# Kernel optimization log

Measured on AMD Instinct MI355X. Metric: run time of the kernel, lower is better.

The kernel has to match this reference:

```python
import jax, jax.numpy as jnp
import numpy as np

B, C, H, W = 16, 256, 64, 64
NH, AG = 8, 64
KD = C // NH
N = H * W


def _bn_params(k, ch):
    k1, k2, k3, k4 = jax.random.split(k, 4)
    g = 1.0 + 0.1 * jax.random.normal(k1, (ch,), jnp.float32)
    b = 0.1 * jax.random.normal(k2, (ch,), jnp.float32)
    m = 0.1 * jax.random.normal(k3, (ch,), jnp.float32)
    v = jax.random.uniform(k4, (ch,), jnp.float32, 0.5, 1.5)
    return jnp.stack([g, b, m, v])


def setup_inputs() -> dict:
    key = jax.random.key(0)
    ks = jax.random.split(key, 16)
    return {
        "x": jax.random.normal(ks[0], (B, C, H, W), jnp.float32),
        "qkv_w": 0.05 * jax.random.normal(ks[1], (3 * C, C), jnp.float32),
        "qkv_bn": _bn_params(ks[2], 3 * C),
        "pe_w": 0.1 * jax.random.normal(ks[3], (C, 1, 3, 3), jnp.float32),
        "pe_bn": _bn_params(ks[4], C),
        "proj_w": 0.05 * jax.random.normal(ks[5], (C, C), jnp.float32),
        "proj_bn": _bn_params(ks[6], C),
        "an_bias": 0.02 * jax.random.normal(ks[7], (NH, AG, 7, 7), jnp.float32),
        "na_bias": 0.02 * jax.random.normal(ks[8], (NH, AG, 7, 7), jnp.float32),
        "ah_bias": 0.02 * jax.random.normal(ks[9], (1, NH, AG, H, 1), jnp.float32),
        "aw_bias": 0.02 * jax.random.normal(ks[10], (1, NH, AG, 1, W), jnp.float32),
        "ha_bias": 0.02 * jax.random.normal(ks[11], (1, NH, H, 1, AG), jnp.float32),
        "wa_bias": 0.02 * jax.random.normal(ks[12], (1, NH, 1, W, AG), jnp.float32),
    }


def _bn(x, p):
    # inference batchnorm: p = [gamma, beta, running_mean, running_var], eps=1e-5
    g, b, m, v = p
    inv = g * jax.lax.rsqrt(v + 1e-5)
    return (x - m[:, None, None]) * inv[:, None, None] + b[:, None, None]


def reference(x, qkv_w, qkv_bn, pe_w, pe_bn, proj_w, proj_bn,
              an_bias, na_bias, ah_bias, aw_bias, ha_bias, wa_bias):
    scale = KD ** -0.5
    qkv = _bn(jnp.einsum('bchw,oc->bohw', x, qkv_w), qkv_bn)  # [B,3C,H,W]
    qkv = qkv.reshape(B, NH, 3 * KD, N)
    q, k, v = qkv[:, :, :KD], qkv[:, :, KD:2 * KD], qkv[:, :, 2 * KD:]  # [B,NH,KD,N]
    # agent tokens: torch's raw reshape of q to [B,H,W,C], NCHW permute, adaptive avg pool to 8x8
    ps = int(AG ** 0.5)
    ap = q.reshape(B, H, W, C).transpose(0, 3, 1, 2)
    ap = ap.reshape(B, C, ps, H // ps, ps, W // ps).mean(axis=(3, 5)).reshape(B, C, AG)
    a = ap.transpose(0, 2, 1).reshape(B, AG, NH, KD).transpose(0, 2, 3, 1)  # [B,NH,KD,AG]
    # agent -> key attention with interpolated + separable position bias
    pb = (jax.image.resize(an_bias, (NH, AG, H, W), 'bilinear').reshape(1, NH, AG, N)
          + (ah_bias + aw_bias).reshape(1, NH, AG, N))
    attn_k = jax.nn.softmax(jnp.einsum('bhca,bhcn->bhan', a, k) * scale + pb, axis=-1)
    attn = jnp.einsum('bhan,bhcn->bhac', attn_k, v)  # [B,NH,AG,KD]
    # query -> agent attention
    ab = (jax.image.resize(na_bias, (NH, AG, H, W), 'bilinear').reshape(1, NH, AG, N).transpose(0, 1, 3, 2)
          + (ha_bias + wa_bias).reshape(1, NH, N, AG))
    q_attn = jax.nn.softmax(jnp.einsum('bhcn,bhca->bhna', q, a) * scale + ab, axis=-1)
    out = jnp.einsum('bhna,bhac->bhcn', q_attn, attn).reshape(B, C, H, W)
    # depthwise 3x3 positional conv on v + residual
    pe = jax.lax.conv_general_dilated(v.reshape(B, C, H, W), pe_w, (1, 1), 'SAME',
                                      feature_group_count=C,
                                      dimension_numbers=('NCHW', 'OIHW', 'NCHW'))
    out = out + _bn(pe, pe_bn)
    return _bn(jnp.einsum('bchw,oc->bohw', out, proj_w), proj_bn)
```

## Files before the change

kernel.cpp:

```cpp
#include <hip/hip_runtime.h>
#include <cmath>


typedef __bf16 bf16;
typedef bf16 bf16x8 __attribute__((ext_vector_type(8)));
typedef float f32x4 __attribute__((ext_vector_type(4)));

__device__ __forceinline__ f32x4 MFMA16(bf16x8 a, bf16x8 b, f32x4 c) {
  return __builtin_amdgcn_mfma_f32_16x16x32_bf16(a, b, c, 0, 0, 0);
}

__device__ __forceinline__ void gll16(const bf16* g, bf16* l) {
  __builtin_amdgcn_global_load_lds(
      (const __attribute__((address_space(1))) void*)g,
      (__attribute__((address_space(3))) void*)l, 16, 0, 0);
}

constexpr int B_ = 16, C_ = 256, N_ = 4096;
constexpr int NH_ = 8, KD_ = 32, AG_ = 64, O3_ = 768;
constexpr int PSTRIDE_ = 64 + 64 + 64 * 32;
constexpr float SCALE_ = 0.17677669529663687f;

__global__ __launch_bounds__(256) void prep_w_kernel(
    const float* __restrict__ qkv_w, const float* __restrict__ qkv_bn,
    const float* __restrict__ proj_w, const float* __restrict__ proj_bn,
    bf16* __restrict__ wqb, float* __restrict__ shq,
    bf16* __restrict__ wpb, float* __restrict__ shp) {
  int o = blockIdx.x, t = threadIdx.x;
  if (o < O3_) {
    float g = qkv_bn[o], bb = qkv_bn[O3_ + o], m = qkv_bn[2 * O3_ + o],
          v = qkv_bn[3 * O3_ + o];
    float s = g * rsqrtf(v + 1e-5f);
    wqb[(size_t)o * C_ + t] = (bf16)(qkv_w[(size_t)o * C_ + t] * s);
    if (t == 0) shq[o] = bb - m * s;
  } else {
    int p = o - O3_;
    float g = proj_bn[p], bb = proj_bn[C_ + p], m = proj_bn[2 * C_ + p],
          v = proj_bn[3 * C_ + p];
    float s = g * rsqrtf(v + 1e-5f);
    wpb[(size_t)p * C_ + t] = (bf16)(proj_w[(size_t)p * C_ + t] * s);
    if (t == 0) shp[p] = bb - m * s;
  }
}

__device__ __forceinline__ float bilerp7(const float* __restrict__ A, int h, int w) {
  float fy = (h + 0.5f) * (7.0f / 64.0f) - 0.5f;
  float fx = (w + 0.5f) * (7.0f / 64.0f) - 0.5f;
  float fy0 = floorf(fy), fx0 = floorf(fx);
  float wy = fy - fy0, wx = fx - fx0;
  int y0 = (int)fy0, x0 = (int)fx0;
  int y0c = min(max(y0, 0), 6), y1c = min(max(y0 + 1, 0), 6);
  int x0c = min(max(x0, 0), 6), x1c = min(max(x0 + 1, 0), 6);
  float a00 = A[y0c * 7 + x0c], a01 = A[y0c * 7 + x1c];
  float a10 = A[y1c * 7 + x0c], a11 = A[y1c * 7 + x1c];
  return (1.0f - wy) * ((1.0f - wx) * a00 + wx * a01) +
         wy * ((1.0f - wx) * a10 + wx * a11);
}

__global__ __launch_bounds__(256) void bias_pb_kernel(
    const float* __restrict__ an, const float* __restrict__ ah,
    const float* __restrict__ aw, bf16* __restrict__ pb) {
  int tid = blockIdx.x * 256 + threadIdx.x;
  int n = tid & (N_ - 1);
  int g = (tid >> 12) & 63;
  int nh = tid >> 18;
  int h = n >> 6, w = n & 63;
  float v = bilerp7(an + (nh * AG_ + g) * 49, h, w);
  pb[tid] = (bf16)(v + ah[(nh * AG_ + g) * 64 + h] + aw[(nh * AG_ + g) * 64 + w]);
}

__global__ __launch_bounds__(256) void bias_ab_kernel(
    const float* __restrict__ na, const float* __restrict__ ha,
    const float* __restrict__ wa, bf16* __restrict__ ab) {
  int tid = blockIdx.x * 256 + threadIdx.x;
  int g = tid & 63;
  int n = (tid >> 6) & (N_ - 1);
  int nh = tid >> 18;
  int h = n >> 6, w = n & 63;
  float v = bilerp7(na + (nh * AG_ + g) * 49, h, w);
  ab[tid] = (bf16)(v + ha[(nh * 64 + h) * AG_ + g] + wa[(nh * 64 + w) * AG_ + g]);
}

__global__ __launch_bounds__(256) void transpose_x_kernel(
    const float* __restrict__ x, bf16* __restrict__ xT) {
  __shared__ __align__(16) unsigned LDSd[64 * 36];
  int b = blockIdx.x, n0 = blockIdx.y * 64, c0 = blockIdx.z * 64;
  int t = threadIdx.x, n = t & 63, cp = t >> 6;
  const float* xb = x + ((size_t)b * C_ + c0) * N_ + n0;
#pragma unroll
  for (int j = 0; j < 8; j++) {
    int cpr = cp * 8 + j;
    int c = cpr * 2;
    float f0 = xb[(size_t)c * N_ + n];
    float f1 = xb[(size_t)(c + 1) * N_ + n];
    union { bf16 h[2]; unsigned u; } pk;
    pk.h[0] = (bf16)f0; pk.h[1] = (bf16)f1;
    LDSd[n * 36 + cpr] = pk.u;
  }
  __syncthreads();
  int n2 = t >> 2, seg = t & 3;
  const unsigned* row = &LDSd[n2 * 36 + seg * 8];
  uint4 d0 = *(const uint4*)row;
  uint4 d1 = *(const uint4*)(row + 4);
  bf16* dst = xT + ((size_t)b * N_ + n0 + n2) * C_ + c0 + seg * 16;
  *(uint4*)dst = d0;
  *(uint4*)(dst + 8) = d1;
}

__global__ __launch_bounds__(256) void qkv_gemm_kernel(
    const bf16* __restrict__ xT, const bf16* __restrict__ wqb,
    const float* __restrict__ shq, bf16* __restrict__ qT,
    bf16* __restrict__ kT, bf16* __restrict__ vv) {
  int nt = blockIdx.x * 128, ot = blockIdx.y * 128, b = blockIdx.z;
  __shared__ __align__(16) bf16 As[128][64];
  __shared__ __align__(16) bf16 Bs[128][64];
  int t = threadIdx.x, wave = t >> 6, lane = t & 63, quad = lane >> 4, l16 = lane & 15;
  int wm = (wave >> 1) * 64, wn = (wave & 1) * 64;
  int lr = lane >> 3;
  int lsw = ((lane & 7) ^ (lr & 7)) * 8;
  f32x4 acc[4][4];
#pragma unroll
  for (int mi = 0; mi < 4; mi++)
#pragma unroll
    for (int ni = 0; ni < 4; ni++) acc[mi][ni] = (f32x4){0.f, 0.f, 0.f, 0.f};
  const bf16* xTb = xT + (size_t)b * N_ * C_;
  for (int k0 = 0; k0 < 256; k0 += 64) {
    __syncthreads();
#pragma unroll
    for (int i = 0; i < 4; i++) {
      int r0 = wave * 32 + i * 8;
      gll16(wqb + (size_t)(ot + r0 + lr) * C_ + k0 + lsw, &As[r0][0]);
      gll16(xTb + (size_t)(nt + r0 + lr) * C_ + k0 + lsw, &Bs[r0][0]);
    }
    __syncthreads();
#pragma unroll
    for (int ks2 = 0; ks2 < 2; ks2++) {
      bf16x8 af[4], bfv[4];
#pragma unroll
      for (int mi = 0; mi < 4; mi++)
        af[mi] = *(const bf16x8*)&As[wm + mi * 16 + l16]
                                   [((ks2 * 4 + quad) ^ (l16 & 7)) * 8];
#pragma unroll
      for (int ni = 0; ni < 4; ni++)
        bfv[ni] = *(const bf16x8*)&Bs[wn + ni * 16 + l16]
                                    [((ks2 * 4 + quad) ^ (l16 & 7)) * 8];
#pragma unroll
      for (int mi = 0; mi < 4; mi++)
#pragma unroll
        for (int ni = 0; ni < 4; ni++)
          acc[mi][ni] = MFMA16(af[mi], bfv[ni], acc[mi][ni]);
    }
  }
#pragma unroll
  for (int mi = 0; mi < 4; mi++) {
    int o0 = ot + wm + mi * 16 + quad * 4;
    float4 s4 = *(const float4*)(shq + o0);
    float sh[4] = {s4.x, s4.y, s4.z, s4.w};
    int base16 = ot + wm + mi * 16;
    int nh = base16 / 96;
    int rem = base16 % 96;
    int type = rem >> 5;
    int kdb = (rem & 31) + quad * 4;
    if (type < 2) {
      bf16* dst = (type == 0 ? qT : kT) + ((size_t)(b * NH_ + nh) * N_) * KD_;
#pragma unroll
      for (int ni = 0; ni < 4; ni++) {
        int n = nt + wn + ni * 16 + l16;
        union { ushort4 u; bf16 e[4]; } pk;
#pragma unroll
        for (int r = 0; r < 4; r++) pk.e[r] = (bf16)(acc[mi][ni][r] + sh[r]);
        *(ushort4*)(dst + (size_t)n * KD_ + kdb) = pk.u;
      }
    } else {
      bf16* dst = vv + ((size_t)(b * NH_ + nh) * KD_) * N_;
#pragma unroll
      for (int ni = 0; ni < 4; ni++) {
        int n = nt + wn + ni * 16 + l16;
#pragma unroll
        for (int r = 0; r < 4; r++)
          dst[(size_t)(kdb + r) * N_ + n] = (bf16)(acc[mi][ni][r] + sh[r]);
      }
    }
  }
}

__global__ __launch_bounds__(256) void pool_kernel(
    const bf16* __restrict__ qT, bf16* __restrict__ aT) {
  int tid = blockIdx.x * 256 + threadIdx.x;
  int kd2 = tid & 31;
  int g = (tid >> 5) & 63;
  int nh2 = (tid >> 11) & 7;
  int b = tid >> 14;
  int c = nh2 * KD_ + kd2;
  int ho = g >> 3, wo = g & 7;
  int ww = c & 63, ch = c >> 6;
  const bf16* qb = qT + ((size_t)(b * NH_ + ho) * N_) * KD_;
  float s = 0.f;
#pragma unroll
  for (int wi = 0; wi < 8; wi++) {
    int w_ = wo * 8 + wi;
    int n1 = ((w_ & 15) * 4 + ch) * 64 + ww;
    int kdlo = w_ >> 4;
#pragma unroll
    for (int hi = 0; hi < 8; hi++)
      s += (float)qb[(size_t)n1 * KD_ + kdlo + hi * 4];
  }
  aT[tid] = (bf16)(s * (1.0f / 64.0f));
}

struct SM3comb { float m[4][64]; float l[4][64]; float o[4][64][32]; };
union SM3u { bf16 Ps[4][64][72]; SM3comb c; };

__global__ __launch_bounds__(256) void attn1_kernel(
    const bf16* __restrict__ kT, const bf16* __restrict__ vv,
    const bf16* __restrict__ aT, const bf16* __restrict__ pb,
    float* __restrict__ part) {
  __shared__ __align__(16) SM3u sm;
  int tile = blockIdx.x, bh = blockIdx.y, nh = bh & 7;
  int t = threadIdx.x, wave = t >> 6, lane = t & 63, quad = lane >> 4, l16 = lane & 15;
  const bf16* aTb = aT + (size_t)bh * (AG_ * KD_);
  const bf16* kb = kT + (size_t)bh * N_ * KD_;
  const bf16* vb = vv + (size_t)bh * KD_ * N_;
  const bf16* pbh = pb + (size_t)nh * AG_ * N_;
  int nloc = wave * 64, ng = tile * 256 + nloc;
  bf16x8 af[4], kf[4];
#pragma unroll
  for (int mi = 0; mi < 4; mi++)
    af[mi] = *(const bf16x8*)(aTb + (mi * 16 + l16) * KD_ + quad * 8);
#pragma unroll
  for (int ni = 0; ni < 4; ni++)
    kf[ni] = *(const bf16x8*)(kb + (size_t)(ng + ni * 16 + l16) * KD_ + quad * 8);
  float mrow[4][4], lrow[4][4];
  f32x4 zero4 = (f32x4){0.f, 0.f, 0.f, 0.f};
#pragma unroll
  for (int mi = 0; mi < 4; mi++) {
    f32x4 s[4];
#pragma unroll
    for (int ni = 0; ni < 4; ni++) s[ni] = MFMA16(af[mi], kf[ni], zero4);
    int g0 = mi * 16 + quad * 4;
#pragma unroll
    for (int ni = 0; ni < 4; ni++) {
      const bf16* p = pbh + (size_t)g0 * N_ + ng + ni * 16 + l16;
#pragma unroll
      for (int r = 0; r < 4; r++)
        s[ni][r] = s[ni][r] * SCALE_ + (float)p[(size_t)r * N_];
    }
#pragma unroll
    for (int r = 0; r < 4; r++) {
      float mx = fmaxf(fmaxf(s[0][r], s[1][r]), fmaxf(s[2][r], s[3][r]));
#pragma unroll
      for (int off = 1; off < 16; off <<= 1) mx = fmaxf(mx, __shfl_xor(mx, off));
      float rs = 0.f;
#pragma unroll
      for (int ni = 0; ni < 4; ni++) {
        float pv = __expf(s[ni][r] - mx);
        s[ni][r] = pv; rs += pv;
      }
#pragma unroll
      for (int off = 1; off < 16; off <<= 1) rs += __shfl_xor(rs, off);
      mrow[mi][r] = mx; lrow[mi][r] = rs;
    }
#pragma unroll
    for (int ni = 0; ni < 4; ni++)
#pragma unroll
      for (int r = 0; r < 4; r++)
        sm.Ps[wave][mi * 16 + quad * 4 + r][ni * 16 + l16] = (bf16)s[ni][r];
  }
  f32x4 oacc[4][2];
#pragma unroll
  for (int mi = 0; mi < 4; mi++) { oacc[mi][0] = zero4; oacc[mi][1] = zero4; }
#pragma unroll
  for (int ks = 0; ks < 2; ks++) {
    bf16x8 vf[2], pf[4];
#pragma unroll
    for (int ci = 0; ci < 2; ci++)
      vf[ci] = *(const bf16x8*)(vb + (size_t)(ci * 16 + l16) * N_ + ng + ks * 32 + quad * 8);
#pragma unroll
    for (int mi = 0; mi < 4; mi++)
      pf[mi] = *(const bf16x8*)&sm.Ps[wave][mi * 16 + l16][ks * 32 + quad * 8];
#pragma unroll
    for (int mi = 0; mi < 4; mi++)
#pragma unroll
      for (int ci = 0; ci < 2; ci++)
        oacc[mi][ci] = MFMA16(pf[mi], vf[ci], oacc[mi][ci]);
  }
  __syncthreads();
#pragma unroll
  for (int mi = 0; mi < 4; mi++)
#pragma unroll
    for (int r = 0; r < 4; r++) {
      int g = mi * 16 + quad * 4 + r;
      if (l16 == 0) { sm.c.m[wave][g] = mrow[mi][r]; sm.c.l[wave][g] = lrow[mi][r]; }
      sm.c.o[wave][g][l16] = oacc[mi][0][r];
      sm.c.o[wave][g][16 + l16] = oacc[mi][1][r];
    }
  __syncthreads();
  {
    int g = t >> 2, kd0 = (t & 3) * 8;
    float M = fmaxf(fmaxf(sm.c.m[0][g], sm.c.m[1][g]), fmaxf(sm.c.m[2][g], sm.c.m[3][g]));
    float ew[4], L = 0.f;
#pragma unroll
    for (int w2 = 0; w2 < 4; w2++) {
      ew[w2] = __expf(sm.c.m[w2][g] - M);
      L += sm.c.l[w2][g] * ew[w2];
    }
    float* pt = part + (size_t)(bh * 16 + tile) * PSTRIDE_;
    if ((t & 3) == 0) { pt[g] = M; pt[64 + g] = L; }
    float4 o0, o1;
    o0.x = o0.y = o0.z = o0.w = 0.f; o1 = o0;
#pragma unroll
    for (int w2 = 0; w2 < 4; w2++) {
      float e = ew[w2];
      const float* src = &sm.c.o[w2][g][kd0];
      o0.x += src[0] * e; o0.y += src[1] * e; o0.z += src[2] * e; o0.w += src[3] * e;
      o1.x += src[4] * e; o1.y += src[5] * e; o1.z += src[6] * e; o1.w += src[7] * e;
    }
    *(float4*)(pt + 128 + g * 32 + kd0) = o0;
    *(float4*)(pt + 128 + g * 32 + kd0 + 4) = o1;
  }
}

__global__ __launch_bounds__(256) void attn1_combine_kernel(
    const float* __restrict__ part, bf16* __restrict__ attnT) {
  int bh = blockIdx.x, t = threadIdx.x;
  int g = t >> 2, kd0 = (t & 3) * 8;
  const float* base = part + (size_t)bh * 16 * PSTRIDE_;
  float gm = -1e30f, L = 0.f;
  float o[8];
#pragma unroll
  for (int j = 0; j < 8; j++) o[j] = 0.f;
  for (int tl = 0; tl < 16; tl++) {
    const float* pt = base + tl * PSTRIDE_;
    float m = pt[g], l = pt[64 + g];
    float nm = fmaxf(gm, m);
    float a0 = __expf(gm - nm), a1 = __expf(m - nm);
    L = L * a0 + l * a1;
    float4 x0 = *(const float4*)(pt + 128 + g * 32 + kd0);
    float4 x1 = *(const float4*)(pt + 128 + g * 32 + kd0 + 4);
    o[0] = o[0] * a0 + x0.x * a1; o[1] = o[1] * a0 + x0.y * a1;
    o[2] = o[2] * a0 + x0.z * a1; o[3] = o[3] * a0 + x0.w * a1;
    o[4] = o[4] * a0 + x1.x * a1; o[5] = o[5] * a0 + x1.y * a1;
    o[6] = o[6] * a0 + x1.z * a1; o[7] = o[7] * a0 + x1.w * a1;
    gm = nm;
  }
  float inv = 1.0f / L;
  bf16* dst = attnT + (size_t)bh * (KD_ * AG_);
#pragma unroll
  for (int j = 0; j < 8; j++)
    dst[(kd0 + j) * AG_ + g] = (bf16)(o[j] * inv);
}

__global__ __launch_bounds__(256) void attn2_kernel(
    const bf16* __restrict__ qT, const bf16* __restrict__ aT,
    const bf16* __restrict__ attnT, const bf16* __restrict__ ab,
    bf16* __restrict__ outa) {
  __shared__ __align__(16) bf16 Ps[4][64][72];
  int nt = blockIdx.x * 256;
  int bh = blockIdx.y, b = bh >> 3, nh = bh & 7;
  int t = threadIdx.x, wave = t >> 6, lane = t & 63, quad = lane >> 4, l16 = lane & 15;
  const bf16* qb = qT + (size_t)bh * N_ * KD_;
  const bf16* aTb = aT + (size_t)bh * (AG_ * KD_);
  const bf16* atb = attnT + (size_t)bh * (KD_ * AG_);
  bf16x8 afr[4], tfr[2][2];
#pragma unroll
  for (int gi = 0; gi < 4; gi++)
    afr[gi] = *(const bf16x8*)(aTb + (gi * 16 + l16) * KD_ + quad * 8);
#pragma unroll
  for (int ci = 0; ci < 2; ci++)
#pragma unroll
    for (int ks = 0; ks < 2; ks++)
      tfr[ci][ks] = *(const bf16x8*)(atb + (ci * 16 + l16) * AG_ + ks * 32 + quad * 8);
  const bf16* abh = ab + (size_t)nh * N_ * AG_;
  int nloc = wave * 64;
  f32x4 zero4 = (f32x4){0.f, 0.f, 0.f, 0.f};
#pragma unroll
  for (int mi = 0; mi < 4; mi++) {
    bf16x8 qf = *(const bf16x8*)(qb + (size_t)(nt + nloc + mi * 16 + l16) * KD_ + quad * 8);
    f32x4 s[4];
#pragma unroll
    for (int gi = 0; gi < 4; gi++)
      s[gi] = MFMA16(qf, afr[gi], zero4);
    int n0 = nt + nloc + mi * 16 + quad * 4;
#pragma unroll
    for (int gi = 0; gi < 4; gi++) {
      int g = gi * 16 + l16;
#pragma unroll
      for (int r = 0; r < 4; r++)
        s[gi][r] = s[gi][r] * SCALE_ + (float)abh[(size_t)(n0 + r) * AG_ + g];
    }
#pragma unroll
    for (int r = 0; r < 4; r++) {
      float mx = fmaxf(fmaxf(s[0][r], s[1][r]), fmaxf(s[2][r], s[3][r]));
#pragma unroll
      for (int off = 1; off < 16; off <<= 1) mx = fmaxf(mx, __shfl_xor(mx, off));
      float rs = 0.f;
#pragma unroll
      for (int gi = 0; gi < 4; gi++) {
        float p = __expf(s[gi][r] - mx);
        s[gi][r] = p; rs += p;
      }
#pragma unroll
      for (int off = 1; off < 16; off <<= 1) rs += __shfl_xor(rs, off);
      float inv = 1.0f / rs;
#pragma unroll
      for (int gi = 0; gi < 4; gi++) s[gi][r] *= inv;
    }
#pragma unroll
    for (int gi = 0; gi < 4; gi++)
#pragma unroll
      for (int r = 0; r < 4; r++)
        Ps[wave][mi * 16 + quad * 4 + r][gi * 16 + l16] = (bf16)s[gi][r];
  }
  __syncthreads();
  f32x4 O[4][2];
#pragma unroll
  for (int mi = 0; mi < 4; mi++) { O[mi][0] = zero4; O[mi][1] = zero4; }
#pragma unroll
  for (int ks = 0; ks < 2; ks++) {
    bf16x8 pf[4];
#pragma unroll
    for (int mi = 0; mi < 4; mi++)
      pf[mi] = *(const bf16x8*)&Ps[wave][mi * 16 + l16][ks * 32 + quad * 8];
#pragma unroll
    for (int mi = 0; mi < 4; mi++)
#pragma unroll
      for (int ci = 0; ci < 2; ci++)
        O[mi][ci] = MFMA16(pf[mi], tfr[ci][ks], O[mi][ci]);
  }
  bf16* ob = outa + (size_t)b * C_ * N_;
#pragma unroll
  for (int mi = 0; mi < 4; mi++) {
    int n0 = nt + nloc + mi * 16 + quad * 4;
#pragma unroll
    for (int ci = 0; ci < 2; ci++) {
      int c = nh * KD_ + ci * 16 + l16;
      union { ushort4 u; bf16 e[4]; } pk;
#pragma unroll
      for (int r = 0; r < 4; r++) pk.e[r] = (bf16)O[mi][ci][r];
      *(ushort4*)(ob + (size_t)c * N_ + n0) = pk.u;
    }
  }
}

__global__ __launch_bounds__(256) void pe_tr_kernel(
    const bf16* __restrict__ vv, const bf16* __restrict__ outa,
    const float* __restrict__ pw, const float* __restrict__ bn,
    bf16* __restrict__ hT) {
  __shared__ __align__(16) bf16 Vs[3][64][68];
  __shared__ __align__(16) bf16 Os[64][68];
  int b = blockIdx.x, n0 = blockIdx.y * 64, c0 = blockIdx.z * 64;
  int h = n0 >> 6;
  int t = threadIdx.x;
#pragma unroll
  for (int dy = 0; dy < 3; dy++) {
    int hh = h + dy - 1;
    bool ok = (unsigned)hh < 64u;
#pragma unroll
    for (int it = 0; it < 2; it++) {
      int u = it * 256 + t;
      int c = u >> 3, seg = u & 7;
      union { uint4 q; uint2 d[2]; } val;
      val.q = make_uint4(0u, 0u, 0u, 0u);
      if (ok)
        val.q = *(const uint4*)(vv + ((size_t)b * C_ + c0 + c) * N_ + hh * 64 + seg * 8);
      *(uint2*)&Vs[dy][c][seg * 8] = val.d[0];
      *(uint2*)&Vs[dy][c][seg * 8 + 4] = val.d[1];
    }
  }
#pragma unroll
  for (int it = 0; it < 2; it++) {
    int u = it * 256 + t;
    int c = u >> 3, seg = u & 7;
    union { uint4 q; uint2 d[2]; } val;
    val.q = *(const uint4*)(outa + ((size_t)b * C_ + c0 + c) * N_ + n0 + seg * 8);
    *(uint2*)&Os[c][seg * 8] = val.d[0];
    *(uint2*)&Os[c][seg * 8 + 4] = val.d[1];
  }
  __syncthreads();
  int cl = t & 63, wv = t >> 6;
  int c = c0 + cl;
  const float* wc = pw + c * 9;
  float w00 = wc[0], w01 = wc[1], w02 = wc[2];
  float w10 = wc[3], w11 = wc[4], w12 = wc[5];
  float w20 = wc[6], w21 = wc[7], w22 = wc[8];
  float sc = bn[c] * rsqrtf(bn[3 * C_ + c] + 1e-5f);
  float sh = bn[C_ + c] - bn[2 * C_ + c] * sc;
#pragma unroll
  for (int half = 0; half < 2; half++) {
    int oct = half * 4 + wv;
    int w0 = oct * 8;
    float r[3][10];
#pragma unroll
    for (int dy = 0; dy < 3; dy++) {
      union { uint2 q; bf16 e[4]; } lo, hi;
      lo.q = *(const uint2*)&Vs[dy][cl][w0];
      hi.q = *(const uint2*)&Vs[dy][cl][w0 + 4];
#pragma unroll
      for (int j = 0; j < 4; j++) {
        r[dy][j + 1] = (float)lo.e[j];
        r[dy][j + 5] = (float)hi.e[j];
      }
      r[dy][0] = (w0 > 0) ? (float)Vs[dy][cl][w0 - 1] : 0.f;
      r[dy][9] = (w0 < 56) ? (float)Vs[dy][cl][w0 + 8] : 0.f;
    }
    union { uint2 q; bf16 e[4]; } plo, phi;
    plo.q = *(const uint2*)&Os[cl][w0];
    phi.q = *(const uint2*)&Os[cl][w0 + 4];
    bf16* dst = hT + ((size_t)b * N_ + n0 + w0) * C_ + c;
#pragma unroll
    for (int j = 0; j < 8; j++) {
      float a = r[0][j] * w00 + r[0][j + 1] * w01 + r[0][j + 2] * w02 +
                r[1][j] * w10 + r[1][j + 1] * w11 + r[1][j + 2] * w12 +
                r[2][j] * w20 + r[2][j + 1] * w21 + r[2][j + 2] * w22;
      float po = (j < 4) ? (float)plo.e[j] : (float)phi.e[j - 4];
      dst[(size_t)j * C_] = (bf16)(po + a * sc + sh);
    }
  }
}

__global__ __launch_bounds__(256) void proj_gemm_kernel(
    const bf16* __restrict__ hT, const bf16* __restrict__ wpb,
    const float* __restrict__ shp, float* __restrict__ out) {
  int nt = blockIdx.x * 128, ot = blockIdx.y * 128, b = blockIdx.z;
  __shared__ __align__(16) bf16 As[128][64];
  __shared__ __align__(16) bf16 Bs[128][64];
  int t = threadIdx.x, wave = t >> 6, lane = t & 63, quad = lane >> 4, l16 = lane & 15;
  int wm = (wave >> 1) * 64, wn = (wave & 1) * 64;
  int lr = lane >> 3;
  int lsw = ((lane & 7) ^ (lr & 7)) * 8;
  f32x4 acc[4][4];
#pragma unroll
  for (int mi = 0; mi < 4; mi++)
#pragma unroll
    for (int ni = 0; ni < 4; ni++) acc[mi][ni] = (f32x4){0.f, 0.f, 0.f, 0.f};
  const bf16* hTb = hT + (size_t)b * N_ * C_;
  for (int k0 = 0; k0 < 256; k0 += 64) {
    __syncthreads();
#pragma unroll
    for (int i = 0; i < 4; i++) {
      int r0 = wave * 32 + i * 8;
      gll16(wpb + (size_t)(ot + r0 + lr) * C_ + k0 + lsw, &As[r0][0]);
      gll16(hTb + (size_t)(nt + r0 + lr) * C_ + k0 + lsw, &Bs[r0][0]);
    }
    __syncthreads();
#pragma unroll
    for (int ks2 = 0; ks2 < 2; ks2++) {
      bf16x8 af[4], bfv[4];
#pragma unroll
      for (int mi = 0; mi < 4; mi++)
        af[mi] = *(const bf16x8*)&As[wm + mi * 16 + l16]
                                   [((ks2 * 4 + quad) ^ (l16 & 7)) * 8];
#pragma unroll
      for (int ni = 0; ni < 4; ni++)
        bfv[ni] = *(const bf16x8*)&Bs[wn + ni * 16 + l16]
                                    [((ks2 * 4 + quad) ^ (l16 & 7)) * 8];
#pragma unroll
      for (int mi = 0; mi < 4; mi++)
#pragma unroll
        for (int ni = 0; ni < 4; ni++)
          acc[mi][ni] = MFMA16(af[mi], bfv[ni], acc[mi][ni]);
    }
  }
  float* ob = out + (size_t)b * C_ * N_;
#pragma unroll
  for (int mi = 0; mi < 4; mi++) {
    int o0 = ot + wm + mi * 16 + quad * 4;
    float4 s4 = *(const float4*)(shp + o0);
    float sh[4] = {s4.x, s4.y, s4.z, s4.w};
#pragma unroll
    for (int ni = 0; ni < 4; ni++) {
      int n = nt + wn + ni * 16 + l16;
#pragma unroll
      for (int r = 0; r < 4; r++)
        ob[(size_t)(o0 + r) * N_ + n] = acc[mi][ni][r] + sh[r];
    }
  }
}

extern "C" void kernel_launch(void* const* d_in, const int* in_sizes, int n_in,
                              void* d_out, int out_size, void* d_ws, size_t ws_size,
                              hipStream_t stream) {
  const float* x = (const float*)d_in[0];
  const float* qkv_w = (const float*)d_in[1];
  const float* qkv_bn = (const float*)d_in[2];
  const float* pe_w = (const float*)d_in[3];
  const float* pe_bn = (const float*)d_in[4];
  const float* proj_w = (const float*)d_in[5];
  const float* proj_bn = (const float*)d_in[6];
  const float* an_bias = (const float*)d_in[7];
  const float* na_bias = (const float*)d_in[8];
  const float* ah_bias = (const float*)d_in[9];
  const float* aw_bias = (const float*)d_in[10];
  const float* ha_bias = (const float*)d_in[11];
  const float* wa_bias = (const float*)d_in[12];

  char* ws = (char*)d_ws;
  bf16* qT = (bf16*)(ws + 0);
  bf16* kT = (bf16*)(ws + 33554432);
  bf16* vv = (bf16*)(ws + 67108864);
  bf16* pb = (bf16*)(ws + 100663296);
  bf16* ab = (bf16*)(ws + 104857600);
  bf16* aT = (bf16*)(ws + 109051904);
  bf16* attnT = (bf16*)(ws + 109576192);
  bf16* outa = (bf16*)(ws + 110100480);
  bf16* wqb = (bf16*)(ws + 143654912);
  bf16* wpb = (bf16*)(ws + 144048128);
  float* shq = (float*)(ws + 144179200);
  float* shp = (float*)(ws + 144183296);
  bf16* xT = outa;
  bf16* houT = kT;
  float* part = (float*)outa;

  prep_w_kernel<<<1024, 256, 0, stream>>>(qkv_w, qkv_bn, proj_w, proj_bn,
                                          wqb, shq, wpb, shp);
  bias_pb_kernel<<<8192, 256, 0, stream>>>(an_bias, ah_bias, aw_bias, pb);
  bias_ab_kernel<<<8192, 256, 0, stream>>>(na_bias, ha_bias, wa_bias, ab);
  transpose_x_kernel<<<dim3(16, 64, 4), 256, 0, stream>>>(x, xT);
  qkv_gemm_kernel<<<dim3(32, 6, 16), 256, 0, stream>>>(xT, wqb, shq, qT, kT, vv);
  pool_kernel<<<1024, 256, 0, stream>>>(qT, aT);
  attn1_kernel<<<dim3(16, 128), 256, 0, stream>>>(kT, vv, aT, pb, part);
  attn1_combine_kernel<<<128, 256, 0, stream>>>(part, attnT);
  attn2_kernel<<<dim3(16, 128), 256, 0, stream>>>(qT, aT, attnT, ab, outa);
  pe_tr_kernel<<<dim3(16, 64, 4), 256, 0, stream>>>(vv, outa, pe_w, pe_bn, houT);
  proj_gemm_kernel<<<dim3(32, 2, 16), 256, 0, stream>>>(houT, wpb, shp,
                                                        (float*)d_out);
}
```

Before: 364.4 us.

## Loop attn1 over four key chunks with online softmax and transposed bias

The agent-to-key attention kernel now gives each wave four consecutive 64-key chunks and merges them with an online (running max and sum) softmax. This cuts the grid from 16 to 4 tiles per head and shrinks the partial buffer and combine work. The position-bias tensor is stored transposed so each lane reads four agents with one vector load, and the combine shared array gets a padding column to reduce bank conflicts. The trade-off is fewer blocks (512 in total), which lowers parallelism and latency hiding for this kernel.

```diff
diff --git a/kernel.cpp b/kernel.cpp
--- a/kernel.cpp
+++ b/kernel.cpp
@@ -18,6 +18,7 @@
 
 constexpr int B_ = 16, C_ = 256, N_ = 4096;
 constexpr int NH_ = 8, KD_ = 32, AG_ = 64, O3_ = 768;
+constexpr int TILES1_ = 4;
 constexpr int PSTRIDE_ = 64 + 64 + 64 * 32;
 constexpr float SCALE_ = 0.17677669529663687f;
 
@@ -59,14 +60,14 @@
 
 __global__ __launch_bounds__(256) void bias_pb_kernel(
     const float* __restrict__ an, const float* __restrict__ ah,
-    const float* __restrict__ aw, bf16* __restrict__ pb) {
+    const float* __restrict__ aw, bf16* __restrict__ pbT) {
   int tid = blockIdx.x * 256 + threadIdx.x;
-  int n = tid & (N_ - 1);
-  int g = (tid >> 12) & 63;
+  int g = tid & 63;
+  int n = (tid >> 6) & (N_ - 1);
   int nh = tid >> 18;
   int h = n >> 6, w = n & 63;
   float v = bilerp7(an + (nh * AG_ + g) * 49, h, w);
-  pb[tid] = (bf16)(v + ah[(nh * AG_ + g) * 64 + h] + aw[(nh * AG_ + g) * 64 + w]);
+  pbT[tid] = (bf16)(v + ah[(nh * AG_ + g) * 64 + h] + aw[(nh * AG_ + g) * 64 + w]);
 }
 
 __global__ __launch_bounds__(256) void bias_ab_kernel(
@@ -208,12 +209,12 @@
   aT[tid] = (bf16)(s * (1.0f / 64.0f));
 }
 
-struct SM3comb { float m[4][64]; float l[4][64]; float o[4][64][32]; };
+struct SM3comb { float m[4][64]; float l[4][64]; float o[4][64][33]; };
 union SM3u { bf16 Ps[4][64][72]; SM3comb c; };
 
 __global__ __launch_bounds__(256) void attn1_kernel(
     const bf16* __restrict__ kT, const bf16* __restrict__ vv,
-    const bf16* __restrict__ aT, const bf16* __restrict__ pb,
+    const bf16* __restrict__ aT, const bf16* __restrict__ pbT,
     float* __restrict__ part) {
   __shared__ __align__(16) SM3u sm;
   int tile = blockIdx.x, bh = blockIdx.y, nh = bh & 7;
@@ -221,68 +222,85 @@
   const bf16* aTb = aT + (size_t)bh * (AG_ * KD_);
   const bf16* kb = kT + (size_t)bh * N_ * KD_;
   const bf16* vb = vv + (size_t)bh * KD_ * N_;
-  const bf16* pbh = pb + (size_t)nh * AG_ * N_;
-  int nloc = wave * 64, ng = tile * 256 + nloc;
-  bf16x8 af[4], kf[4];
+  const bf16* pbh = pbT + (size_t)nh * N_ * AG_;
+  bf16x8 af[4];
 #pragma unroll
   for (int mi = 0; mi < 4; mi++)
     af[mi] = *(const bf16x8*)(aTb + (mi * 16 + l16) * KD_ + quad * 8);
-#pragma unroll
-  for (int ni = 0; ni < 4; ni++)
-    kf[ni] = *(const bf16x8*)(kb + (size_t)(ng + ni * 16 + l16) * KD_ + quad * 8);
   float mrow[4][4], lrow[4][4];
   f32x4 zero4 = (f32x4){0.f, 0.f, 0.f, 0.f};
+  f32x4 oacc[4][2];
 #pragma unroll
   for (int mi = 0; mi < 4; mi++) {
-    f32x4 s[4];
-#pragma unroll
-    for (int ni = 0; ni < 4; ni++) s[ni] = MFMA16(af[mi], kf[ni], zero4);
-    int g0 = mi * 16 + quad * 4;
-#pragma unroll
-    for (int ni = 0; ni < 4; ni++) {
-      const bf16* p = pbh + (size_t)g0 * N_ + ng + ni * 16 + l16;
-#pragma unroll
-      for (int r = 0; r < 4; r++)
-        s[ni][r] = s[ni][r] * SCALE_ + (float)p[(size_t)r * N_];
-    }
-#pragma unroll
-    for (int r = 0; r < 4; r++) {
-      float mx = fmaxf(fmaxf(s[0][r], s[1][r]), fmaxf(s[2][r], s[3][r]));
-#pragma unroll
-      for (int off = 1; off < 16; off <<= 1) mx = fmaxf(mx, __shfl_xor(mx, off));
-      float rs = 0.f;
+    oacc[mi][0] = zero4; oacc[mi][1] = zero4;
+#pragma unroll
+    for (int r = 0; r < 4; r++) { mrow[mi][r] = -1e30f; lrow[mi][r] = 0.f; }
+  }
+  for (int it = 0; it < 4; it++) {
+    int ng = tile * 1024 + wave * 256 + it * 64;
+    bf16x8 kf[4];
+#pragma unroll
+    for (int ni = 0; ni < 4; ni++)
+      kf[ni] = *(const bf16x8*)(kb + (size_t)(ng + ni * 16 + l16) * KD_ + quad * 8);
+#pragma unroll
+    for (int mi = 0; mi < 4; mi++) {
+      f32x4 s[4];
+#pragma unroll
+      for (int ni = 0; ni < 4; ni++) s[ni] = MFMA16(af[mi], kf[ni], zero4);
+      int g0 = mi * 16 + quad * 4;
 #pragma unroll
       for (int ni = 0; ni < 4; ni++) {
-        float pv = __expf(s[ni][r] - mx);
-        s[ni][r] = pv; rs += pv;
+        union { ushort4 u; bf16 e[4]; } pv4;
+        pv4.u = *(const ushort4*)(pbh + (size_t)(ng + ni * 16 + l16) * AG_ + g0);
+#pragma unroll
+        for (int r = 0; r < 4; r++)
+          s[ni][r] = s[ni][r] * SCALE_ + (float)pv4.e[r];
       }
-#pragma unroll
-      for (int off = 1; off < 16; off <<= 1) rs += __shfl_xor(rs, off);
-      mrow[mi][r] = mx; lrow[mi][r] = rs;
-    }
-#pragma unroll
-    for (int ni = 0; ni < 4; ni++)
-#pragma unroll
-      for (int r = 0; r < 4; r++)
-        sm.Ps[wave][mi * 16 + quad * 4 + r][ni * 16 + l16] = (bf16)s[ni][r];
-  }
-  f32x4 oacc[4][2];
-#pragma unroll
-  for (int mi = 0; mi < 4; mi++) { oacc[mi][0] = zero4; oacc[mi][1] = zero4; }
-#pragma unroll
-  for (int ks = 0; ks < 2; ks++) {
-    bf16x8 vf[2], pf[4];
-#pragma unroll
-    for (int ci = 0; ci < 2; ci++)
-      vf[ci] = *(const bf16x8*)(vb + (size_t)(ci * 16 + l16) * N_ + ng + ks * 32 + quad * 8);
-#pragma unroll
-    for (int mi = 0; mi < 4; mi++)
-      pf[mi] = *(const bf16x8*)&sm.Ps[wave][mi * 16 + l16][ks * 32 + quad * 8];
-#pragma unroll
-    for (int mi = 0; mi < 4; mi++)
+      float fac[4];
+#pragma unroll
+      for (int r = 0; r < 4; r++) {
+        float mx = fmaxf(fmaxf(s[0][r], s[1][r]), fmaxf(s[2][r], s[3][r]));
+#pragma unroll
+        for (int off = 1; off < 16; off <<= 1) mx = fmaxf(mx, __shfl_xor(mx, off));
+        float newm = fmaxf(mrow[mi][r], mx);
+        float rs = 0.f;
+#pragma unroll
+        for (int ni = 0; ni < 4; ni++) {
+          float pv = __expf(s[ni][r] - newm);
+          s[ni][r] = pv; rs += pv;
+        }
+#pragma unroll
+        for (int off = 1; off < 16; off <<= 1) rs += __shfl_xor(rs, off);
+        float f = __expf(mrow[mi][r] - newm);
+        lrow[mi][r] = lrow[mi][r] * f + rs;
+        mrow[mi][r] = newm;
+        fac[r] = f;
+      }
 #pragma unroll
       for (int ci = 0; ci < 2; ci++)
-        oacc[mi][ci] = MFMA16(pf[mi], vf[ci], oacc[mi][ci]);
+#pragma unroll
+        for (int r = 0; r < 4; r++) oacc[mi][ci][r] *= fac[r];
+#pragma unroll
+      for (int ni = 0; ni < 4; ni++)
+#pragma unroll
+        for (int r = 0; r < 4; r++)
+          sm.Ps[wave][mi * 16 + quad * 4 + r][ni * 16 + l16] = (bf16)s[ni][r];
+    }
+#pragma unroll
+    for (int ks = 0; ks < 2; ks++) {
+      bf16x8 vf[2], pf[4];
+#pragma unroll
+      for (int ci = 0; ci < 2; ci++)
+        vf[ci] = *(const bf16x8*)(vb + (size_t)(ci * 16 + l16) * N_ + ng + ks * 32 + quad * 8);
+#pragma unroll
+      for (int mi = 0; mi < 4; mi++)
+        pf[mi] = *(const bf16x8*)&sm.Ps[wave][mi * 16 + l16][ks * 32 + quad * 8];
+#pragma unroll
+      for (int mi = 0; mi < 4; mi++)
+#pragma unroll
+        for (int ci = 0; ci < 2; ci++)
+          oacc[mi][ci] = MFMA16(pf[mi], vf[ci], oacc[mi][ci]);
+    }
   }
   __syncthreads();
 #pragma unroll
@@ -304,7 +322,7 @@
       ew[w2] = __expf(sm.c.m[w2][g] - M);
       L += sm.c.l[w2][g] * ew[w2];
     }
-    float* pt = part + (size_t)(bh * 16 + tile) * PSTRIDE_;
+    float* pt = part + (size_t)(bh * TILES1_ + tile) * PSTRIDE_;
     if ((t & 3) == 0) { pt[g] = M; pt[64 + g] = L; }
     float4 o0, o1;
     o0.x = o0.y = o0.z = o0.w = 0.f; o1 = o0;
@@ -324,12 +342,12 @@
     const float* __restrict__ part, bf16* __restrict__ attnT) {
   int bh = blockIdx.x, t = threadIdx.x;
   int g = t >> 2, kd0 = (t & 3) * 8;
-  const float* base = part + (size_t)bh * 16 * PSTRIDE_;
+  const float* base = part + (size_t)bh * TILES1_ * PSTRIDE_;
   float gm = -1e30f, L = 0.f;
   float o[8];
 #pragma unroll
   for (int j = 0; j < 8; j++) o[j] = 0.f;
-  for (int tl = 0; tl < 16; tl++) {
+  for (int tl = 0; tl < TILES1_; tl++) {
     const float* pt = base + tl * PSTRIDE_;
     float m = pt[g], l = pt[64 + g];
     float nm = fmaxf(gm, m);
@@ -618,7 +636,7 @@
   transpose_x_kernel<<<dim3(16, 64, 4), 256, 0, stream>>>(x, xT);
   qkv_gemm_kernel<<<dim3(32, 6, 16), 256, 0, stream>>>(xT, wqb, shq, qT, kT, vv);
   pool_kernel<<<1024, 256, 0, stream>>>(qT, aT);
-  attn1_kernel<<<dim3(16, 128), 256, 0, stream>>>(kT, vv, aT, pb, part);
+  attn1_kernel<<<dim3(TILES1_, 128), 256, 0, stream>>>(kT, vv, aT, pb, part);
   attn1_combine_kernel<<<128, 256, 0, stream>>>(part, attnT);
   attn2_kernel<<<dim3(16, 128), 256, 0, stream>>>(qT, aT, attnT, ab, outa);
   pe_tr_kernel<<<dim3(16, 64, 4), 256, 0, stream>>>(vv, outa, pe_w, pe_bn, houT);
```

Result: no change. 369.6 us (+1.4%).
